# Optimization experiments

Measured on AMD Instinct MI355X. Metric: run time of the kernel, lower is better.

The kernel has to match this reference:

```python
import jax, jax.numpy as jnp
import numpy as np

HEADS = 16
D_K = 64  # hidden_size // heads = 1024 // 16
SCALE = D_K ** 0.5


def setup_inputs() -> dict:
    key = jax.random.key(0)
    ks = jax.random.split(key, 7)
    B, S, D = 4, 2048, 1024
    H = 1024  # hidden_size
    O = 1024  # outputs_dims
    s = 0.02
    return {
        "query": jax.random.normal(ks[0], (B, S, D), dtype=jnp.float32),
        "key": jax.random.normal(ks[1], (B, S, D), dtype=jnp.float32),
        "value": jax.random.normal(ks[2], (B, S, D), dtype=jnp.float32),
        "Wq": jax.random.normal(ks[3], (D, H), dtype=jnp.float32) * s,
        "Wk": jax.random.normal(ks[4], (D, H), dtype=jnp.float32) * s,
        "Wv": jax.random.normal(ks[5], (D, H), dtype=jnp.float32) * s,
        "Wo": jax.random.normal(ks[6], (H, O), dtype=jnp.float32) * s,
    }


def reference(query, key, value, Wq, Wk, Wv, Wo):
    B, S, _ = query.shape
    # Dense projections with relu activation (as in the original module)
    q = jax.nn.relu(query @ Wq).reshape(B, S, HEADS, D_K)  # [B,S,H,dk]
    k = jax.nn.relu(key @ Wk).reshape(B, S, HEADS, D_K)
    v = jax.nn.relu(value @ Wv).reshape(B, S, HEADS, D_K)
    # scores: [B,H,Sq,Sk]
    scores = jnp.einsum('bqhd,bkhd->bhqk', q, k) / SCALE
    attn = jax.nn.softmax(scores, axis=-1)
    # attention-weighted values -> [B,Sq,H,dk] -> [B,Sq,H*dk]
    ctx = jnp.einsum('bhqk,bkhd->bqhd', attn, v).reshape(B, S, HEADS * D_K)
    out = jax.nn.relu(ctx @ Wo)
    return out
```

## Files before the change

### kernel.cpp

```cpp
#include <hip/hip_runtime.h>

typedef unsigned short u16;
typedef __bf16 bf16x8 __attribute__((ext_vector_type(8)));
typedef float f32x4 __attribute__((ext_vector_type(4)));
typedef u16 u16x8 __attribute__((ext_vector_type(8)));
typedef u16 u16x4 __attribute__((ext_vector_type(4)));

#define MFMA16(a, b, c) __builtin_amdgcn_mfma_f32_16x16x32_bf16(a, b, c, 0, 0, 0)

static constexpr float QSC = 0.18033688011112042f;

__device__ inline u16 f2bf(float f) {
  union { float f; unsigned u; } x; x.f = f;
  unsigned r = x.u + 0x7FFF + ((x.u >> 16) & 1);
  return (u16)(r >> 16);
}
__device__ inline u16 cvt_bf(float f) {
  __bf16 h = (__bf16)f; return __builtin_bit_cast(u16, h);
}
__device__ inline bf16x8 ld_frag(const u16* p) {
  return __builtin_bit_cast(bf16x8, *(const u16x8*)p);
}
__device__ inline void dma16(const u16* g, u16* l) {
  __builtin_amdgcn_global_load_lds(
      (const __attribute__((address_space(1))) unsigned*)g,
      (__attribute__((address_space(3))) unsigned*)l, 16, 0, 0);
}

#if __has_builtin(__builtin_amdgcn_exp2f)
#define EXP2(x) __builtin_amdgcn_exp2f(x)
#else
#define EXP2(x) exp2f(x)
#endif

__launch_bounds__(256)
__global__ void prep_w(const float* __restrict__ Wq, const float* __restrict__ Wk,
                       const float* __restrict__ Wv, const float* __restrict__ Wo,
                       u16* __restrict__ Wt) {
  __shared__ u16 T[64 * 72];
  const int z = blockIdx.z;
  const float* W = z == 0 ? Wq : z == 1 ? Wk : z == 2 ? Wv : Wo;
  u16* D = Wt + ((size_t)z << 20);
  const int k0 = blockIdx.y * 64, c0 = blockIdx.x * 64;
  const int tid = threadIdx.x;
  const int kr = tid >> 2, cs = (tid & 3) * 16;
  const float* src = W + (size_t)(k0 + kr) * 1024 + c0 + cs;
  float f[16];
#pragma unroll
  for (int i = 0; i < 4; ++i) *(float4*)&f[i * 4] = ((const float4*)src)[i];
#pragma unroll
  for (int i = 0; i < 16; ++i) T[(cs + i) * 72 + kr] = cvt_bf(f[i]);
  __syncthreads();
  const int nn = tid >> 2, ks = (tid & 3) * 16;
  u16* dst = D + (size_t)(c0 + nn) * 1024 + k0 + ks;
  *(u16x8*)dst = *(u16x8*)&T[nn * 72 + ks];
  *(u16x8*)(dst + 8) = *(u16x8*)&T[nn * 72 + ks + 8];
}

__launch_bounds__(256)
__global__ void prep_a(const float* __restrict__ q, const float* __restrict__ k,
                       const float* __restrict__ v, u16* __restrict__ dq,
                       u16* __restrict__ dk, u16* __restrict__ dv) {
  const int z = blockIdx.z;
  const float* s = z == 0 ? q : z == 1 ? k : v;
  u16* d = z == 0 ? dq : z == 1 ? dk : dv;
  for (size_t i = blockIdx.x * 256 + threadIdx.x; i < (size_t)1048576; i += 262144) {
    const float* g = s + i * 8;
    float4 f0 = *(const float4*)g, f1 = *(const float4*)(g + 4);
    u16x8 h;
    h[0] = cvt_bf(f0.x); h[1] = cvt_bf(f0.y); h[2] = cvt_bf(f0.z); h[3] = cvt_bf(f0.w);
    h[4] = cvt_bf(f1.x); h[5] = cvt_bf(f1.y); h[6] = cvt_bf(f1.z); h[7] = cvt_bf(f1.w);
    *(u16x8*)(d + i * 8) = h;
  }
}

__launch_bounds__(512, 2)
__global__ void gemm_fwd(const u16* __restrict__ Aq, const u16* __restrict__ Ak,
                         const u16* __restrict__ Av, const u16* __restrict__ Wt,
                         u16* __restrict__ Qw, u16* __restrict__ Kw,
                         u16* __restrict__ Vw) {
  __shared__ u16 smem[65536];
  const int z = blockIdx.z;
  const u16* A = z == 0 ? Aq : z == 1 ? Ak : Av;
  const u16* Bt = Wt + ((size_t)z << 20);
  u16* out = z == 0 ? Qw : z == 1 ? Kw : Vw;
  const u16* Aop = (z == 2) ? Bt : A;
  const u16* Bop = (z == 2) ? A : Bt;

  const int tid = threadIdx.x;
  const int lane = tid & 63, l15 = lane & 15, quad = lane >> 4;
  const int wv = tid >> 6, wm = wv & 1, wn = wv >> 1;
  const int mblk = ((blockIdx.x & 7) << 2) | (blockIdx.x >> 3);
  const int m0 = (z == 2) ? blockIdx.y * 256 : mblk * 256;
  const int n0 = (z == 2) ? mblk * 256 : blockIdx.y * 256;

  const u16* gA[4];
  const u16* gB[4];
#pragma unroll
  for (int i = 0; i < 4; ++i) {
    const int c = i * 512 + tid;
    gA[i] = Aop + (size_t)(m0 + (c & 255)) * 1024 + (c >> 8) * 8;
    gB[i] = Bop + (size_t)(n0 + (c & 255)) * 1024 + (c >> 8) * 8;
  }

  const int offA = (quad * 256 + wm * 128 + l15) * 8;
  const int offB = 16384 + (quad * 256 + wn * 64 + l15) * 8;

  f32x4 acc[8][4] = {};

#pragma unroll
  for (int i = 0; i < 4; ++i) dma16(gA[i], &smem[i * 4096 + wv * 512]);
#pragma unroll
  for (int i = 0; i < 4; ++i) dma16(gB[i], &smem[16384 + i * 4096 + wv * 512]);
  asm volatile("s_waitcnt vmcnt(0)" ::: "memory");
  __builtin_amdgcn_sched_barrier(0);
  __builtin_amdgcn_s_barrier();

#pragma unroll 1
  for (int t = 0; t < 16; ++t) {
    const int bo = (t & 1) ? 32768 : 0;
    const int nbo = bo ^ 32768;
    bf16x8 a[4], b[4];
    if (t < 15) {
#pragma unroll
      for (int i = 0; i < 4; ++i)
        dma16(gA[i] + (t + 1) * 64, &smem[nbo + i * 4096 + wv * 512]);
    }
#pragma unroll
    for (int j = 0; j < 4; ++j) b[j] = ld_frag(&smem[bo + offB + j * 128]);
#pragma unroll
    for (int i = 0; i < 4; ++i) a[i] = ld_frag(&smem[bo + offA + i * 128]);
    asm volatile("s_waitcnt lgkmcnt(0)" ::: "memory");
    __builtin_amdgcn_sched_barrier(0);
    __builtin_amdgcn_s_setprio(1);
#pragma unroll
    for (int i = 0; i < 4; ++i)
#pragma unroll
      for (int j = 0; j < 4; ++j)
        acc[i][j] = MFMA16(a[i], b[j], acc[i][j]);
    __builtin_amdgcn_s_setprio(0);
#pragma unroll
    for (int i = 0; i < 4; ++i)
      a[i] = ld_frag(&smem[bo + offA + (4 + i) * 128]);
    asm volatile("s_waitcnt lgkmcnt(0)" ::: "memory");
    __builtin_amdgcn_sched_barrier(0);
    __builtin_amdgcn_s_setprio(1);
#pragma unroll
    for (int i = 0; i < 4; ++i)
#pragma unroll
      for (int j = 0; j < 4; ++j)
        acc[4 + i][j] = MFMA16(a[i], b[j], acc[4 + i][j]);
    __builtin_amdgcn_s_setprio(0);
    if (t < 15) {
#pragma unroll
      for (int i = 0; i < 4; ++i)
        dma16(gB[i] + (t + 1) * 64, &smem[nbo + 16384 + i * 4096 + wv * 512]);
    }
#pragma unroll
    for (int j = 0; j < 4; ++j)
      b[j] = ld_frag(&smem[bo + offB + 8192 + j * 128]);
#pragma unroll
    for (int i = 0; i < 4; ++i)
      a[i] = ld_frag(&smem[bo + offA + 8192 + i * 128]);
    asm volatile("s_waitcnt lgkmcnt(0)" ::: "memory");
    __builtin_amdgcn_sched_barrier(0);
    __builtin_amdgcn_s_setprio(1);
#pragma unroll
    for (int i = 0; i < 4; ++i)
#pragma unroll
      for (int j = 0; j < 4; ++j)
        acc[i][j] = MFMA16(a[i], b[j], acc[i][j]);
    __builtin_amdgcn_s_setprio(0);
#pragma unroll
    for (int i = 0; i < 4; ++i)
      a[i] = ld_frag(&smem[bo + offA + 8192 + (4 + i) * 128]);
    asm volatile("s_waitcnt lgkmcnt(0)" ::: "memory");
    __builtin_amdgcn_sched_barrier(0);
    __builtin_amdgcn_s_setprio(1);
#pragma unroll
    for (int i = 0; i < 4; ++i)
#pragma unroll
      for (int j = 0; j < 4; ++j)
        acc[4 + i][j] = MFMA16(a[i], b[j], acc[4 + i][j]);
    __builtin_amdgcn_s_setprio(0);
    if (t < 15) {
      asm volatile("s_waitcnt vmcnt(0)" ::: "memory");
      __builtin_amdgcn_sched_barrier(0);
    }
    __builtin_amdgcn_s_barrier();
  }

  if (z < 2) {
    const float sc = z == 0 ? QSC : 1.0f;
#pragma unroll
    for (int i = 0; i < 8; ++i)
#pragma unroll
      for (int j = 0; j < 4; ++j)
#pragma unroll
        for (int r = 0; r < 4; ++r) {
          float v = fmaxf(acc[i][j][r], 0.f) * sc;
          int m = m0 + wm * 128 + i * 16 + quad * 4 + r;
          int n = n0 + wn * 64 + j * 16 + l15;
          out[(size_t)m * 1024 + n] = f2bf(v);
        }
  } else {
    const int bb = n0 >> 11, s0 = n0 & 2047;
#pragma unroll
    for (int half = 0; half < 2; ++half) {
      __syncthreads();
      if ((wn >> 1) == half) {
#pragma unroll
        for (int i = 0; i < 8; ++i)
#pragma unroll
          for (int j = 0; j < 4; ++j)
#pragma unroll
            for (int r = 0; r < 4; ++r) {
              const int row = wm * 128 + i * 16 + quad * 4 + r;
              const int col = (wn & 1) * 64 + j * 16 + l15;
              smem[row * 128 + col] = f2bf(fmaxf(acc[i][j][r], 0.f));
            }
      }
      __syncthreads();
#pragma unroll
      for (int i2 = 0; i2 < 8; ++i2) {
        const int c = i2 * 512 + tid;
        const int row = c >> 4, ch = c & 15;
        u16* dst = out + (size_t)(bb * 1024 + m0 + row) * 2048 + s0 +
                   half * 128 + ch * 8;
        *(u16x8*)dst = *(u16x8*)&smem[row * 128 + ch * 8];
      }
    }
  }
}

__launch_bounds__(256, 2)
__global__ void gemm_out(const u16* __restrict__ A, const u16* __restrict__ Bt,
                         float* __restrict__ out) {
  __shared__ u16 smem[49152];
  const int tid = threadIdx.x;
  const int lane = tid & 63, l15 = lane & 15, quad = lane >> 4;
  const int wv = tid >> 6, wm = wv & 1, wn = wv >> 1;
  const int mblk = ((blockIdx.x & 7) << 2) | (blockIdx.x >> 3);
  const int m0 = mblk * 256;
  const int n0 = blockIdx.y * 128;

  const u16* gA[8];
#pragma unroll
  for (int i = 0; i < 8; ++i) {
    const int c = i * 256 + tid;
    gA[i] = A + (size_t)(m0 + (c & 255)) * 1024 + (c >> 8) * 8;
  }
  const u16* gB[4];
#pragma unroll
  for (int i = 0; i < 4; ++i) {
    const int c = i * 256 + tid;
    gB[i] = Bt + (size_t)(n0 + (c & 127)) * 1024 + (c >> 7) * 8;
  }

  const int offA = (quad * 256 + wm * 128 + l15) * 8;
  const int offB = 16384 + (quad * 128 + wn * 64 + l15) * 8;

  f32x4 acc[8][4] = {};

#pragma unroll
  for (int i = 0; i < 8; ++i) dma16(gA[i], &smem[i * 2048 + wv * 512]);
#pragma unroll
  for (int i = 0; i < 4; ++i) dma16(gB[i], &smem[16384 + i * 2048 + wv * 512]);
  asm volatile("s_waitcnt vmcnt(0)" ::: "memory");
  __builtin_amdgcn_sched_barrier(0);
  __builtin_amdgcn_s_barrier();

#pragma unroll 1
  for (int t = 0; t < 16; ++t) {
    const int bo = (t & 1) ? 24576 : 0;
    const int nbo = bo ^ 24576;
    bf16x8 a[4], b[4];
    if (t < 15) {
#pragma unroll
      for (int i = 0; i < 8; ++i)
        dma16(gA[i] + (t + 1) * 64, &smem[nbo + i * 2048 + wv * 512]);
    }
#pragma unroll
    for (int j = 0; j < 4; ++j) b[j] = ld_frag(&smem[bo + offB + j * 128]);
#pragma unroll
    for (int i = 0; i < 4; ++i) a[i] = ld_frag(&smem[bo + offA + i * 128]);
    asm volatile("s_waitcnt lgkmcnt(0)" ::: "memory");
    __builtin_amdgcn_sched_barrier(0);
    __builtin_amdgcn_s_setprio(1);
#pragma unroll
    for (int i = 0; i < 4; ++i)
#pragma unroll
      for (int j = 0; j < 4; ++j)
        acc[i][j] = MFMA16(a[i], b[j], acc[i][j]);
    __builtin_amdgcn_s_setprio(0);
#pragma unroll
    for (int i = 0; i < 4; ++i)
      a[i] = ld_frag(&smem[bo + offA + (4 + i) * 128]);
    asm volatile("s_waitcnt lgkmcnt(0)" ::: "memory");
    __builtin_amdgcn_sched_barrier(0);
    __builtin_amdgcn_s_setprio(1);
#pragma unroll
    for (int i = 0; i < 4; ++i)
#pragma unroll
      for (int j = 0; j < 4; ++j)
        acc[4 + i][j] = MFMA16(a[i], b[j], acc[4 + i][j]);
    __builtin_amdgcn_s_setprio(0);
    if (t < 15) {
#pragma unroll
      for (int i = 0; i < 4; ++i)
        dma16(gB[i] + (t + 1) * 64, &smem[nbo + 16384 + i * 2048 + wv * 512]);
    }
#pragma unroll
    for (int j = 0; j < 4; ++j)
      b[j] = ld_frag(&smem[bo + offB + 4096 + j * 128]);
#pragma unroll
    for (int i = 0; i < 4; ++i)
      a[i] = ld_frag(&smem[bo + offA + 8192 + i * 128]);
    asm volatile("s_waitcnt lgkmcnt(0)" ::: "memory");
    __builtin_amdgcn_sched_barrier(0);
    __builtin_amdgcn_s_setprio(1);
#pragma unroll
    for (int i = 0; i < 4; ++i)
#pragma unroll
      for (int j = 0; j < 4; ++j)
        acc[i][j] = MFMA16(a[i], b[j], acc[i][j]);
    __builtin_amdgcn_s_setprio(0);
#pragma unroll
    for (int i = 0; i < 4; ++i)
      a[i] = ld_frag(&smem[bo + offA + 8192 + (4 + i) * 128]);
    asm volatile("s_waitcnt lgkmcnt(0)" ::: "memory");
    __builtin_amdgcn_sched_barrier(0);
    __builtin_amdgcn_s_setprio(1);
#pragma unroll
    for (int i = 0; i < 4; ++i)
#pragma unroll
      for (int j = 0; j < 4; ++j)
        acc[4 + i][j] = MFMA16(a[i], b[j], acc[4 + i][j]);
    __builtin_amdgcn_s_setprio(0);
    if (t < 15) {
      asm volatile("s_waitcnt vmcnt(0)" ::: "memory");
      __builtin_amdgcn_sched_barrier(0);
    }
    __builtin_amdgcn_s_barrier();
  }

#pragma unroll
  for (int i = 0; i < 8; ++i)
#pragma unroll
    for (int j = 0; j < 4; ++j)
#pragma unroll
      for (int r = 0; r < 4; ++r) {
        int m = m0 + wm * 128 + i * 16 + quad * 4 + r;
        int n = n0 + wn * 64 + j * 16 + l15;
        out[(size_t)m * 1024 + n] = fmaxf(acc[i][j][r], 0.f);
      }
}

__launch_bounds__(256, 2)
__global__ void attn(const u16* __restrict__ Q, const u16* __restrict__ K,
                     const u16* __restrict__ V, u16* __restrict__ ctx) {
  __shared__ u16 Ksm[2][4096];
  __shared__ u16 Vsm[2][4096];
  __shared__ u16 Psm[4][4096];

  const int tid = threadIdx.x;
  const int lane = tid & 63, l15 = lane & 15, quad = lane >> 4;
  const int wv = tid >> 6;
  const int bh = blockIdx.x, b = bh >> 4, h = bh & 15;
  const int q0 = blockIdx.y * 256 + wv * 64;

  const u16* Kb = K + ((size_t)b * 2048) * 1024 + h * 64;
  const u16* Vb = V + (size_t)bh * 64 * 2048;
  u16* Pw = Psm[wv];

  const int ck0 = tid, ck1 = 256 + tid;
  const u16* kg0 = Kb + (size_t)(ck0 & 63) * 1024 + (ck0 >> 6) * 8;
  const u16* kg1 = Kb + (size_t)(ck1 & 63) * 1024 + (ck1 >> 6) * 8;
  const u16* vg0 = Vb + (size_t)(ck0 & 63) * 2048 + (ck0 >> 6) * 8;
  const u16* vg1 = Vb + (size_t)(ck1 & 63) * 2048 + (ck1 >> 6) * 8;

  bf16x8 aq[4][2];
#pragma unroll
  for (int qh = 0; qh < 4; ++qh)
#pragma unroll
    for (int kk = 0; kk < 2; ++kk)
      aq[qh][kk] = ld_frag(Q + (size_t)(b * 2048 + q0 + qh * 16 + l15) * 1024 +
                           h * 64 + kk * 32 + quad * 8);

  f32x4 o[4][4] = {};
  float ls[4] = {0.f, 0.f, 0.f, 0.f};

  dma16(kg0, &Ksm[0][ck0 * 8]);
  dma16(kg1, &Ksm[0][ck1 * 8]);
  dma16(vg0, &Vsm[0][ck0 * 8]);
  dma16(vg1, &Vsm[0][ck1 * 8]);

#pragma unroll 1
  for (int t = 0; t < 32; ++t) {
    const int cur = t & 1, nxt = cur ^ 1;
    __syncthreads();

    if (t + 1 < 32) {
      const int kadv = (t + 1) * 64;
      dma16(kg0 + (size_t)kadv * 1024, &Ksm[nxt][ck0 * 8]);
      dma16(kg1 + (size_t)kadv * 1024, &Ksm[nxt][ck1 * 8]);
      dma16(vg0 + kadv, &Vsm[nxt][ck0 * 8]);
      dma16(vg1 + kadv, &Vsm[nxt][ck1 * 8]);
    }

    bf16x8 kf[2][4];
#pragma unroll
    for (int kk = 0; kk < 2; ++kk)
#pragma unroll
      for (int jj = 0; jj < 4; ++jj)
        kf[kk][jj] = ld_frag(&Ksm[cur][((kk * 4 + quad) * 64 + jj * 16 + l15) * 8]);

    f32x4 st[4][4] = {};
    asm volatile("s_waitcnt lgkmcnt(0)" ::: "memory");
    __builtin_amdgcn_sched_barrier(0);
    __builtin_amdgcn_s_setprio(1);
#pragma unroll
    for (int kk = 0; kk < 2; ++kk)
#pragma unroll
      for (int jj = 0; jj < 4; ++jj)
#pragma unroll
        for (int qh = 0; qh < 4; ++qh)
          st[qh][jj] = MFMA16(kf[kk][jj], aq[qh][kk], st[qh][jj]);
    __builtin_amdgcn_s_setprio(0);

#pragma unroll
    for (int qh = 0; qh < 4; ++qh)
#pragma unroll
      for (int jj = 0; jj < 4; ++jj) {
        float p0 = EXP2(st[qh][jj][0]), p1 = EXP2(st[qh][jj][1]);
        float p2 = EXP2(st[qh][jj][2]), p3 = EXP2(st[qh][jj][3]);
        ls[qh] += (p0 + p1) + (p2 + p3);
        u16x4 pk;
        pk[0] = cvt_bf(p0); pk[1] = cvt_bf(p1);
        pk[2] = cvt_bf(p2); pk[3] = cvt_bf(p3);
        const int kc = jj * 2 + (quad >> 1);
        *(u16x4*)&Pw[(kc * 64 + qh * 16 + l15) * 8 + (quad & 1) * 4] = pk;
      }

#pragma unroll
    for (int kk = 0; kk < 2; ++kk) {
      bf16x8 pa[4];
#pragma unroll
      for (int qh = 0; qh < 4; ++qh)
        pa[qh] = ld_frag(&Pw[((kk * 4 + quad) * 64 + qh * 16 + l15) * 8]);
      asm volatile("s_waitcnt lgkmcnt(0)" ::: "memory");
      __builtin_amdgcn_sched_barrier(0);
      __builtin_amdgcn_s_setprio(1);
#pragma unroll
      for (int j = 0; j < 4; ++j) {
        bf16x8 vb = ld_frag(&Vsm[cur][((kk * 4 + quad) * 64 + j * 16 + l15) * 8]);
#pragma unroll
        for (int qh = 0; qh < 4; ++qh)
          o[qh][j] = MFMA16(vb, pa[qh], o[qh][j]);
      }
      __builtin_amdgcn_s_setprio(0);
    }
  }

  float inv[4];
#pragma unroll
  for (int qh = 0; qh < 4; ++qh) {
    ls[qh] += __shfl_xor(ls[qh], 16, 64);
    ls[qh] += __shfl_xor(ls[qh], 32, 64);
    inv[qh] = 1.f / ls[qh];
  }

#pragma unroll
  for (int qh = 0; qh < 4; ++qh) {
    const int tok = b * 2048 + q0 + qh * 16 + l15;
#pragma unroll
    for (int j = 0; j < 4; ++j) {
      u16x4 pk;
#pragma unroll
      for (int r = 0; r < 4; ++r) pk[r] = cvt_bf(o[qh][j][r] * inv[qh]);
      *(u16x4*)&ctx[(size_t)tok * 1024 + h * 64 + j * 16 + quad * 4] = pk;
    }
  }
}

extern "C" void kernel_launch(void* const* d_in, const int* in_sizes, int n_in,
                              void* d_out, int out_size, void* d_ws, size_t ws_size,
                              hipStream_t stream) {
  const float* query = (const float*)d_in[0];
  const float* key   = (const float*)d_in[1];
  const float* value = (const float*)d_in[2];
  const float* Wq = (const float*)d_in[3];
  const float* Wk = (const float*)d_in[4];
  const float* Wv = (const float*)d_in[5];
  const float* Wo = (const float*)d_in[6];
  float* outp = (float*)d_out;

  u16* Wt  = (u16*)d_ws;
  u16* Awq = Wt + ((size_t)4 << 20);
  u16* Qw  = Awq + ((size_t)8 << 20);
  u16* Kw  = Qw + ((size_t)8 << 20);
  u16* Vt  = Kw + ((size_t)8 << 20);
  u16* Awk = (u16*)d_out;
  u16* Awv = Awk + ((size_t)8 << 20);
  u16* Cw  = Awq;

  prep_w<<<dim3(16, 16, 4), 256, 0, stream>>>(Wq, Wk, Wv, Wo, Wt);
  prep_a<<<dim3(1024, 1, 3), 256, 0, stream>>>(query, key, value, Awq, Awk, Awv);
  gemm_fwd<<<dim3(32, 4, 3), 512, 0, stream>>>(Awq, Awk, Awv, Wt, Qw, Kw, Vt);
  attn<<<dim3(64, 8), 256, 0, stream>>>(Qw, Kw, Vt, Cw);
  gemm_out<<<dim3(32, 8), 256, 0, stream>>>(Cw, Wt + ((size_t)3 << 20), outp);
}
```

Before: 364.7 us.

## Restructure projection GEMM mainloop into finer-grained interleaved DMA and MFMA phases

Reworks the QKV projection GEMM main loop so each K-tile is split into two 32-wide halves, with global-to-LDS DMA issued in smaller chunks interleaved between four MFMA phases and partial vmcnt waits. B fragments for both halves are kept in registers (bk0/bk1) so A sub-tiles can be reused across them. The LDS layout changes so A and B halves live in separate 8192-element regions. The aim is to overlap loads with compute more evenly and keep MFMA fed, at the cost of more barriers per iteration and extra register pressure.

Result: no change. 360.5 us (-1.1%).

```diff
diff --git a/kernel.cpp b/kernel.cpp
--- a/kernel.cpp
+++ b/kernel.cpp
@@ -94,97 +94,124 @@
   const int m0 = (z == 2) ? blockIdx.y * 256 : mblk * 256;
   const int n0 = (z == 2) ? mblk * 256 : blockIdx.y * 256;
 
-  const u16* gA[4];
-  const u16* gB[4];
-#pragma unroll
-  for (int i = 0; i < 4; ++i) {
+  const u16* gA[2];
+  const u16* gB[2];
+#pragma unroll
+  for (int i = 0; i < 2; ++i) {
     const int c = i * 512 + tid;
     gA[i] = Aop + (size_t)(m0 + (c & 255)) * 1024 + (c >> 8) * 8;
     gB[i] = Bop + (size_t)(n0 + (c & 255)) * 1024 + (c >> 8) * 8;
   }
+  const int ub0 = (wv * 64) * 8, ub1 = (512 + wv * 64) * 8;
 
   const int offA = (quad * 256 + wm * 128 + l15) * 8;
-  const int offB = 16384 + (quad * 256 + wn * 64 + l15) * 8;
+  const int offB = (quad * 256 + wn * 64 + l15) * 8;
 
   f32x4 acc[8][4] = {};
 
 #pragma unroll
-  for (int i = 0; i < 4; ++i) dma16(gA[i], &smem[i * 4096 + wv * 512]);
-#pragma unroll
-  for (int i = 0; i < 4; ++i) dma16(gB[i], &smem[16384 + i * 4096 + wv * 512]);
+  for (int h = 0; h < 2; ++h) {
+    dma16(gA[0] + h * 32, &smem[h * 8192 + ub0]);
+    dma16(gA[1] + h * 32, &smem[h * 8192 + ub1]);
+    dma16(gB[0] + h * 32, &smem[16384 + h * 8192 + ub0]);
+    dma16(gB[1] + h * 32, &smem[16384 + h * 8192 + ub1]);
+  }
   asm volatile("s_waitcnt vmcnt(0)" ::: "memory");
   __builtin_amdgcn_sched_barrier(0);
   __builtin_amdgcn_s_barrier();
 
 #pragma unroll 1
   for (int t = 0; t < 16; ++t) {
-    const int bo = (t & 1) ? 32768 : 0;
-    const int nbo = bo ^ 32768;
-    bf16x8 a[4], b[4];
-    if (t < 15) {
-#pragma unroll
-      for (int i = 0; i < 4; ++i)
-        dma16(gA[i] + (t + 1) * 64, &smem[nbo + i * 4096 + wv * 512]);
-    }
-#pragma unroll
-    for (int j = 0; j < 4; ++j) b[j] = ld_frag(&smem[bo + offB + j * 128]);
-#pragma unroll
-    for (int i = 0; i < 4; ++i) a[i] = ld_frag(&smem[bo + offA + i * 128]);
-    asm volatile("s_waitcnt lgkmcnt(0)" ::: "memory");
-    __builtin_amdgcn_sched_barrier(0);
-    __builtin_amdgcn_s_setprio(1);
-#pragma unroll
-    for (int i = 0; i < 4; ++i)
-#pragma unroll
-      for (int j = 0; j < 4; ++j)
-        acc[i][j] = MFMA16(a[i], b[j], acc[i][j]);
-    __builtin_amdgcn_s_setprio(0);
-#pragma unroll
-    for (int i = 0; i < 4; ++i)
-      a[i] = ld_frag(&smem[bo + offA + (4 + i) * 128]);
-    asm volatile("s_waitcnt lgkmcnt(0)" ::: "memory");
-    __builtin_amdgcn_sched_barrier(0);
-    __builtin_amdgcn_s_setprio(1);
-#pragma unroll
-    for (int i = 0; i < 4; ++i)
-#pragma unroll
-      for (int j = 0; j < 4; ++j)
-        acc[4 + i][j] = MFMA16(a[i], b[j], acc[4 + i][j]);
-    __builtin_amdgcn_s_setprio(0);
-    if (t < 15) {
-#pragma unroll
-      for (int i = 0; i < 4; ++i)
-        dma16(gB[i] + (t + 1) * 64, &smem[nbo + 16384 + i * 4096 + wv * 512]);
-    }
-#pragma unroll
-    for (int j = 0; j < 4; ++j)
-      b[j] = ld_frag(&smem[bo + offB + 8192 + j * 128]);
-#pragma unroll
-    for (int i = 0; i < 4; ++i)
-      a[i] = ld_frag(&smem[bo + offA + 8192 + i * 128]);
-    asm volatile("s_waitcnt lgkmcnt(0)" ::: "memory");
-    __builtin_amdgcn_sched_barrier(0);
-    __builtin_amdgcn_s_setprio(1);
-#pragma unroll
-    for (int i = 0; i < 4; ++i)
-#pragma unroll
-      for (int j = 0; j < 4; ++j)
-        acc[i][j] = MFMA16(a[i], b[j], acc[i][j]);
-    __builtin_amdgcn_s_setprio(0);
-#pragma unroll
-    for (int i = 0; i < 4; ++i)
-      a[i] = ld_frag(&smem[bo + offA + 8192 + (4 + i) * 128]);
-    asm volatile("s_waitcnt lgkmcnt(0)" ::: "memory");
-    __builtin_amdgcn_sched_barrier(0);
-    __builtin_amdgcn_s_setprio(1);
-#pragma unroll
-    for (int i = 0; i < 4; ++i)
-#pragma unroll
-      for (int j = 0; j < 4; ++j)
-        acc[4 + i][j] = MFMA16(a[i], b[j], acc[4 + i][j]);
-    __builtin_amdgcn_s_setprio(0);
-    if (t < 15) {
+    const int pb = (t & 1) * 32768;
+    const int nb = 32768 - pb;
+    const u16* aB = smem + pb;
+    const u16* bB = smem + pb + 16384;
+    u16* nA = smem + nb;
+    u16* nBf = smem + nb + 16384;
+    const int adv = (t + 1) * 64;
+    bf16x8 bk0[4], bk1[4], a[4];
+
+#pragma unroll
+    for (int j = 0; j < 4; ++j) bk0[j] = ld_frag(bB + offB + j * 128);
+#pragma unroll
+    for (int i = 0; i < 4; ++i) a[i] = ld_frag(aB + offA + i * 128);
+    if (t < 15) {
+      dma16(gA[0] + adv, &nA[ub0]);
+      dma16(gA[1] + adv, &nA[ub1]);
+    }
+    __builtin_amdgcn_s_barrier();
+    asm volatile("s_waitcnt lgkmcnt(0)" ::: "memory");
+    __builtin_amdgcn_sched_barrier(0);
+    __builtin_amdgcn_s_setprio(1);
+#pragma unroll
+    for (int i = 0; i < 4; ++i)
+#pragma unroll
+      for (int j = 0; j < 4; ++j)
+        acc[i][j] = MFMA16(a[i], bk0[j], acc[i][j]);
+    __builtin_amdgcn_s_setprio(0);
+    if (t < 15)
+      asm volatile("s_waitcnt vmcnt(2)" ::: "memory");
+    else
       asm volatile("s_waitcnt vmcnt(0)" ::: "memory");
+    __builtin_amdgcn_sched_barrier(0);
+    __builtin_amdgcn_s_barrier();
+
+#pragma unroll
+    for (int j = 0; j < 4; ++j) bk1[j] = ld_frag(bB + offB + 8192 + j * 128);
+#pragma unroll
+    for (int i = 0; i < 4; ++i) a[i] = ld_frag(aB + offA + 8192 + i * 128);
+    if (t < 15) {
+      dma16(gB[0] + adv, &nBf[ub0]);
+      dma16(gB[1] + adv, &nBf[ub1]);
+    }
+    __builtin_amdgcn_s_barrier();
+    asm volatile("s_waitcnt lgkmcnt(0)" ::: "memory");
+    __builtin_amdgcn_sched_barrier(0);
+    __builtin_amdgcn_s_setprio(1);
+#pragma unroll
+    for (int i = 0; i < 4; ++i)
+#pragma unroll
+      for (int j = 0; j < 4; ++j)
+        acc[i][j] = MFMA16(a[i], bk1[j], acc[i][j]);
+    __builtin_amdgcn_s_setprio(0);
+    __builtin_amdgcn_s_barrier();
+
+#pragma unroll
+    for (int i = 0; i < 4; ++i) a[i] = ld_frag(aB + offA + (4 + i) * 128);
+    if (t < 15) {
+      dma16(gA[0] + adv + 32, &nA[8192 + ub0]);
+      dma16(gA[1] + adv + 32, &nA[8192 + ub1]);
+    }
+    __builtin_amdgcn_s_barrier();
+    asm volatile("s_waitcnt lgkmcnt(0)" ::: "memory");
+    __builtin_amdgcn_sched_barrier(0);
+    __builtin_amdgcn_s_setprio(1);
+#pragma unroll
+    for (int i = 0; i < 4; ++i)
+#pragma unroll
+      for (int j = 0; j < 4; ++j)
+        acc[4 + i][j] = MFMA16(a[i], bk0[j], acc[4 + i][j]);
+    __builtin_amdgcn_s_setprio(0);
+    __builtin_amdgcn_s_barrier();
+
+#pragma unroll
+    for (int i = 0; i < 4; ++i) a[i] = ld_frag(aB + offA + 8192 + (4 + i) * 128);
+    if (t < 15) {
+      dma16(gB[0] + adv + 32, &nBf[8192 + ub0]);
+      dma16(gB[1] + adv + 32, &nBf[8192 + ub1]);
+    }
+    __builtin_amdgcn_s_barrier();
+    asm volatile("s_waitcnt lgkmcnt(0)" ::: "memory");
+    __builtin_amdgcn_sched_barrier(0);
+    __builtin_amdgcn_s_setprio(1);
+#pragma unroll
+    for (int i = 0; i < 4; ++i)
+#pragma unroll
+      for (int j = 0; j < 4; ++j)
+        acc[4 + i][j] = MFMA16(a[i], bk1[j], acc[4 + i][j]);
+    __builtin_amdgcn_s_setprio(0);
+    if (t < 15) {
+      asm volatile("s_waitcnt vmcnt(4)" ::: "memory");
       __builtin_amdgcn_sched_barrier(0);
     }
     __builtin_amdgcn_s_barrier();
```
